# Kernel tuning notes

Hardware: AMD Instinct MI355X
Metric: run time of the kernel (lower is better)

The kernel has to match this reference:

```python
import jax, jax.numpy as jnp
import numpy as np

B, CIN, COUT, K, SDIM, H, W = 16, 512, 512, 3, 512, 64, 64


def setup_inputs() -> dict:
    key = jax.random.key(0)
    k1, k2, k3, k4 = jax.random.split(key, 4)
    return {
        "x": jax.random.normal(k1, (B, CIN, H, W), dtype=jnp.float32),
        "style": jax.random.normal(k2, (B, SDIM), dtype=jnp.float32),
        "weight": jax.random.normal(k3, (COUT, CIN, K, K), dtype=jnp.float32),
        "style_w": jax.random.normal(k4, (CIN, SDIM), dtype=jnp.float32),
        "style_b": jnp.ones((CIN,), dtype=jnp.float32),  # bias.data.fill_(1.0)
    }


def reference(x, style, weight, style_w, style_b):
    batch, in_ch, h, w_size = x.shape
    out_ch, _, ks, _ = weight.shape
    pad = ks // 2
    # EqualizedLinear: runtime weight scaling by 1/sqrt(fan_in)
    lin_scale = 1.0 / np.sqrt(style_w.shape[1])
    s = style @ (style_w * lin_scale).T + style_b  # [B, Cin]
    # modulate
    conv_scale = 1.0 / np.sqrt(in_ch * ks * ks)
    wmod = (weight[None] * conv_scale) * s[:, None, :, None, None]  # [B,Cout,Cin,k,k]
    # demodulate
    dcoef = jax.lax.rsqrt(jnp.sum(jnp.square(wmod), axis=(2, 3, 4)) + 1e-8)  # [B,Cout]
    wmod = wmod * dcoef[:, :, None, None, None]
    # grouped conv with groups = batch
    x_r = x.reshape(1, batch * in_ch, h, w_size)
    w_r = wmod.reshape(batch * out_ch, in_ch, ks, ks)
    out = jax.lax.conv_general_dilated(
        x_r, w_r,
        window_strides=(1, 1),
        padding=[(pad, pad), (pad, pad)],
        dimension_numbers=("NCHW", "OIHW", "NCHW"),
        feature_group_count=batch,
    )
    return out.reshape(batch, out_ch, h, w_size)
```

## Files before the change

kernel.cpp:

```cpp
#include <hip/hip_runtime.h>
#include <math.h>

#define B 16
#define CIN 512
#define COUT 512
#define SDIM 512
#define H 64
#define W 64

typedef short s16x8 __attribute__((ext_vector_type(8)));
typedef float f32x4 __attribute__((ext_vector_type(4)));

__device__ __constant__ float LIN_SCALE  = 0.04419417382415922f;
__device__ __constant__ float CONV_SCALE = 0.014731391274719742f;

__device__ __forceinline__ ushort f2bf(float f) {
  unsigned u = __float_as_uint(f);
  return (ushort)((u + 0x7FFFu + ((u >> 16) & 1u)) >> 16);
}

#define GLOAD16(g, l)                                           \
  __builtin_amdgcn_global_load_lds(                             \
      (const __attribute__((address_space(1))) unsigned*)(g),   \
      (__attribute__((address_space(3))) unsigned*)(l), 16, 0, 0)

__global__ __launch_bounds__(512) void style_mod_kernel(
    const float* __restrict__ style, const float* __restrict__ style_w,
    const float* __restrict__ style_b, float* __restrict__ s,
    float* __restrict__ s2) {
  const int b = blockIdx.x;
  const int ci = threadIdx.x;
  __shared__ float st[SDIM];
  st[ci] = style[b * SDIM + ci];
  __syncthreads();

  const float4* wr = reinterpret_cast<const float4*>(style_w + (size_t)ci * SDIM);
  float acc = 0.f;
#pragma unroll 4
  for (int k = 0; k < SDIM / 4; ++k) {
    float4 wv = wr[k];
    acc += st[4 * k + 0] * wv.x + st[4 * k + 1] * wv.y +
           st[4 * k + 2] * wv.z + st[4 * k + 3] * wv.w;
  }
  float v = acc * LIN_SCALE + style_b[ci];
  s[b * CIN + ci] = v;
  s2[b * CIN + ci] = v * v;
}

__global__ __launch_bounds__(256) void wsq_kernel(
    const float* __restrict__ weight, float* __restrict__ wsq) {
  const int i = blockIdx.x * blockDim.x + threadIdx.x;
  if (i >= COUT * CIN) return;
  const float* p = weight + (size_t)i * 9;
  float a = 0.f;
#pragma unroll
  for (int k = 0; k < 9; ++k) {
    float v = p[k];
    a += v * v;
  }
  wsq[i] = a;
}

__global__ __launch_bounds__(512) void dcoef_kernel(
    const float* __restrict__ s2, const float* __restrict__ wsq,
    float* __restrict__ outscale) {
  const int b = blockIdx.x;
  const int co = threadIdx.x;
  __shared__ float sh[CIN];
  sh[co] = s2[b * CIN + co];
  __syncthreads();

  const float4* wr = reinterpret_cast<const float4*>(wsq + (size_t)co * CIN);
  float acc = 0.f;
#pragma unroll 4
  for (int k = 0; k < CIN / 4; ++k) {
    float4 wv = wr[k];
    acc += sh[4 * k + 0] * wv.x + sh[4 * k + 1] * wv.y +
           sh[4 * k + 2] * wv.z + sh[4 * k + 3] * wv.w;
  }
  float d = rsqrtf(acc * CONV_SCALE * CONV_SCALE + 1e-8f);
  outscale[b * COUT + co] = d * CONV_SCALE;
}

__global__ __launch_bounds__(256) void pack_w_kernel(
    const float* __restrict__ w, ushort* __restrict__ wt) {
  const int t = blockIdx.x * 256 + threadIdx.x;
  const int s = t & 3;
  const int chunk = (t >> 2) & 15;
  const int co = t >> 6;
  const float4* wp =
      (const float4*)(w + ((size_t)co * 512 + chunk * 32 + s * 8) * 9);
  float wv[72];
#pragma unroll
  for (int i = 0; i < 18; ++i) {
    float4 v = wp[i];
    wv[4 * i + 0] = v.x; wv[4 * i + 1] = v.y;
    wv[4 * i + 2] = v.z; wv[4 * i + 3] = v.w;
  }
  const int sp = s ^ ((co >> 1) & 3);
  ushort* dst = wt + (size_t)chunk * 147456 + (size_t)co * 32 + sp * 8;
#pragma unroll
  for (int j = 0; j < 9; ++j) {
    s16x8 p;
#pragma unroll
    for (int i = 0; i < 8; ++i) p[i] = (short)f2bf(wv[i * 9 + j]);
    *(s16x8*)(dst + (size_t)j * 16384) = p;
  }
}

__global__ __launch_bounds__(256) void pack_x_kernel(
    const float* __restrict__ x, const float* __restrict__ smod,
    ushort* __restrict__ xp) {
  __shared__ float xt[32][65];
  __shared__ float sm[32];
  const int tid = threadIdx.x;
  const int gr = blockIdx.x, chunk = blockIdx.y, b = blockIdx.z;
  if (tid < 32) sm[tid] = smod[b * 512 + chunk * 32 + tid];
  {
    const int ci = tid >> 3, cq = tid & 7;
    const float4* rp = (const float4*)(
        x + (((size_t)b * 512 + chunk * 32 + ci) * 64 + gr) * 64 + cq * 8);
    float4 a = rp[0], c2 = rp[1];
    float* row = &xt[ci][cq * 8];
    row[0] = a.x; row[1] = a.y; row[2] = a.z; row[3] = a.w;
    row[4] = c2.x; row[5] = c2.y; row[6] = c2.z; row[7] = c2.w;
  }
  __syncthreads();
  const int c = tid >> 2, s = tid & 3;
  s16x8 p;
#pragma unroll
  for (int i = 0; i < 8; ++i)
    p[i] = (short)f2bf(xt[s * 8 + i][c] * sm[s * 8 + i]);
  const int sp = s ^ (((c + 1) >> 1) & 3);
  *(s16x8*)(xp + ((size_t)(b * 16 + chunk) * 64 + gr) * 2048 + c * 32 + sp * 8) = p;
}

#define WSBUF 36864
#define XSBUF 42240
#define XSOFF 73728

__global__ __launch_bounds__(512, 2) void conv_mfma3_kernel(
    const ushort* __restrict__ wt, const ushort* __restrict__ xp,
    const float* __restrict__ outscale, float* __restrict__ out) {
  extern __shared__ char smem[];

  const int tid = threadIdx.x;
  const int hb = blockIdx.x;
  const int cb = blockIdx.y;
  const int b  = blockIdx.z;
  const int h0 = hb * 8, co0 = cb * 64;
  const int lane = tid & 63, wid = tid >> 6;
  const int l15 = lane & 15, l4 = lane >> 4;

  {
    s16x8* p = (s16x8*)(smem + XSOFF);
    for (int e = tid; e < (2 * XSBUF) / 16; e += 512) p[e] = (s16x8)0;
  }

  f32x4 acc[4][4];
#pragma unroll
  for (int mt = 0; mt < 4; ++mt)
#pragma unroll
    for (int nt = 0; nt < 4; ++nt) acc[mt][nt] = (f32x4)0.f;

  const int am = (l4 ^ ((l15 >> 1) & 3)) * 16;
  int aoff[4];
#pragma unroll
  for (int mt = 0; mt < 4; ++mt) aoff[mt] = (mt * 16 + l15) * 64 + am;
  int boff[12];
#pragma unroll
  for (int nt = 0; nt < 4; ++nt)
#pragma unroll
    for (int kw = 0; kw < 3; ++kw) {
      int col = nt * 16 + l15 + kw;
      boff[nt * 3 + kw] =
          wid * 4224 + col * 64 + ((l4 ^ ((col >> 1) & 3)) * 16);
    }

  const char* wsrc0 = (const char*)wt + cb * 4096 + lane * 16;
  const char* xsrc0 = (const char*)xp + (size_t)b * 4194304 + lane * 16;

  __syncthreads();

  auto stage = [&](int chunk, int buf) {
    const char* wsrc = wsrc0 + (size_t)chunk * 294912;
    const char* xsrc = xsrc0 + (size_t)chunk * 262144;
    char* wdst = smem + buf * WSBUF + lane * 16;
    char* xdst = smem + XSOFF + buf * XSBUF + 64 + lane * 16;
    for (int e = wid; e < 76; e += 8) {
      if (e < 36) {
        int j = e >> 2, q = e & 3;
        GLOAD16(wsrc + j * 32768 + q * 1024, wdst + j * 4096 + q * 1024);
      } else {
        int r = (e - 36) >> 2, q = (e - 36) & 3;
        int gr = h0 - 1 + r;
        if ((unsigned)gr < 64u)
          GLOAD16(xsrc + (size_t)gr * 4096 + q * 1024,
                  xdst + r * 4224 + q * 1024);
      }
    }
  };

  auto compute = [&](int buf) {
    const char* wb = smem + buf * WSBUF;
    const char* xb = smem + XSOFF + buf * XSBUF;
#pragma unroll
    for (int kh = 0; kh < 3; ++kh) {
      const char* xrow = xb + kh * 4224;
#pragma unroll
      for (int kw = 0; kw < 3; ++kw) {
        const int j = kh * 3 + kw;
        const char* wj = wb + j * 4096;
        s16x8 af[4], bf[4];
#pragma unroll
        for (int mt = 0; mt < 4; ++mt)
          af[mt] = *(const s16x8*)(wj + aoff[mt]);
#pragma unroll
        for (int nt = 0; nt < 4; ++nt)
          bf[nt] = *(const s16x8*)(xrow + boff[nt * 3 + kw]);
#pragma unroll
        for (int mt = 0; mt < 4; ++mt)
#pragma unroll
          for (int nt = 0; nt < 4; ++nt)
            acc[mt][nt] = __builtin_amdgcn_mfma_f32_16x16x32_bf16(
                af[mt], bf[nt], acc[mt][nt], 0, 0, 0);
      }
    }
  };

  stage(0, 0);
  for (int c = 0; c < 16; c += 2) {
    __syncthreads();
    if (c + 1 < 16) stage(c + 1, 1);
    compute(0);
    __syncthreads();
    if (c + 2 < 16) stage(c + 2, 0);
    compute(1);
  }

  const int h = h0 + wid;
#pragma unroll
  for (int mt = 0; mt < 4; ++mt) {
#pragma unroll
    for (int r = 0; r < 4; ++r) {
      const int co = co0 + mt * 16 + l4 * 4 + r;
      const float osc = outscale[b * COUT + co];
      float* orow = out + (((size_t)b * COUT + co) * H + h) * W;
#pragma unroll
      for (int nt = 0; nt < 4; ++nt)
        orow[nt * 16 + l15] = acc[mt][nt][r] * osc;
    }
  }
}

__global__ __launch_bounds__(256, 2) void conv_mfma2_kernel(
    const ushort* __restrict__ wt, const ushort* __restrict__ xp,
    const float* __restrict__ outscale, float* __restrict__ out) {
  __shared__ ushort ws[9][64][32];
  __shared__ ushort xs[6][66][32];

  const int tid = threadIdx.x;
  const int hb = blockIdx.x, cb = blockIdx.y, b = blockIdx.z;
  const int h0 = hb * 4, co0 = cb * 64;
  const int lane = tid & 63, wid = tid >> 6;
  const int l15 = lane & 15, l4 = lane >> 4;

  {
    s16x8* p = (s16x8*)&xs[0][0][0];
    for (int e = tid; e < 1584; e += 256) p[e] = (s16x8)0;
  }

  f32x4 acc[4][4];
#pragma unroll
  for (int mt = 0; mt < 4; ++mt)
#pragma unroll
    for (int nt = 0; nt < 4; ++nt) acc[mt][nt] = (f32x4)0.f;

  const int am = (l4 ^ ((l15 >> 1) & 3)) * 16;
  int aoff[4];
#pragma unroll
  for (int mt = 0; mt < 4; ++mt) aoff[mt] = (mt * 16 + l15) * 64 + am;
  int boff[12];
#pragma unroll
  for (int nt = 0; nt < 4; ++nt)
#pragma unroll
    for (int kw = 0; kw < 3; ++kw) {
      int col = nt * 16 + l15 + kw;
      boff[nt * 3 + kw] =
          wid * 4224 + col * 64 + ((l4 ^ ((col >> 1) & 3)) * 16);
    }

  const char* wsrc0 = (const char*)wt + cb * 4096 + wid * 1024 + lane * 16;
  const char* xsrc0 =
      (const char*)xp + (size_t)b * 4194304 + wid * 1024 + lane * 16;
  char* wdst = (char*)&ws[0][0][0] + wid * 1024 + lane * 16;
  char* xdst = (char*)&xs[0][0][0] + 64 + wid * 1024 + lane * 16;

  __syncthreads();

  for (int chunk = 0; chunk < 16; ++chunk) {
    const char* wsrc = wsrc0 + chunk * 294912;
    const char* xsrc = xsrc0 + chunk * 262144;
#pragma unroll
    for (int t = 0; t < 9; ++t)
      GLOAD16(wsrc + t * 32768, wdst + t * 4096);
#pragma unroll
    for (int t = 0; t < 6; ++t) {
      int gr = h0 - 1 + t;
      if ((unsigned)gr < 64u) GLOAD16(xsrc + gr * 4096, xdst + t * 4224);
    }
    __syncthreads();

#pragma unroll
    for (int kh = 0; kh < 3; ++kh) {
      const char* xrow = (const char*)&xs[0][0][0] + kh * 4224;
#pragma unroll
      for (int kw = 0; kw < 3; ++kw) {
        const int j = kh * 3 + kw;
        const char* wj = (const char*)&ws[0][0][0] + j * 4096;
        s16x8 af[4], bf[4];
#pragma unroll
        for (int mt = 0; mt < 4; ++mt)
          af[mt] = *(const s16x8*)(wj + aoff[mt]);
#pragma unroll
        for (int nt = 0; nt < 4; ++nt)
          bf[nt] = *(const s16x8*)(xrow + boff[nt * 3 + kw]);
#pragma unroll
        for (int mt = 0; mt < 4; ++mt)
#pragma unroll
          for (int nt = 0; nt < 4; ++nt)
            acc[mt][nt] = __builtin_amdgcn_mfma_f32_16x16x32_bf16(
                af[mt], bf[nt], acc[mt][nt], 0, 0, 0);
      }
    }
    __syncthreads();
  }

  const int h = h0 + wid;
#pragma unroll
  for (int mt = 0; mt < 4; ++mt) {
#pragma unroll
    for (int r = 0; r < 4; ++r) {
      const int co = co0 + mt * 16 + l4 * 4 + r;
      const float osc = outscale[b * COUT + co];
      float* orow = out + (((size_t)b * COUT + co) * H + h) * W;
#pragma unroll
      for (int nt = 0; nt < 4; ++nt)
        orow[nt * 16 + l15] = acc[mt][nt][r] * osc;
    }
  }
}

extern "C" void kernel_launch(void* const* d_in, const int* in_sizes, int n_in,
                              void* d_out, int out_size, void* d_ws,
                              size_t ws_size, hipStream_t stream) {
  const float* x = (const float*)d_in[0];
  const float* style = (const float*)d_in[1];
  const float* weight = (const float*)d_in[2];
  const float* style_w = (const float*)d_in[3];
  const float* style_b = (const float*)d_in[4];
  float* out = (float*)d_out;

  char* wsb = (char*)d_ws;
  float* s = (float*)(wsb + 0);
  float* s2 = (float*)(wsb + 32768);
  float* wsq = (float*)(wsb + 65536);
  float* outscale = (float*)(wsb + 1114112);
  ushort* wt = (ushort*)(wsb + 1146880);
  ushort* xp = (ushort*)(wsb + 5865472);
  const size_t NEED = 72974336;

  style_mod_kernel<<<B, 512, 0, stream>>>(style, style_w, style_b, s, s2);
  wsq_kernel<<<(COUT * CIN + 255) / 256, 256, 0, stream>>>(weight, wsq);
  dcoef_kernel<<<B, 512, 0, stream>>>(s2, wsq, outscale);

  pack_w_kernel<<<128, 256, 0, stream>>>(weight, wt);
  pack_x_kernel<<<dim3(64, 16, 16), 256, 0, stream>>>(x, s, xp);

  const int DLDS = 2 * WSBUF + 2 * XSBUF;
  static_assert(2 * WSBUF + 2 * XSBUF == 158208, "lds layout");
  hipError_t attr_ok = hipFuncSetAttribute(
      reinterpret_cast<const void*>(conv_mfma3_kernel),
      hipFuncAttributeMaxDynamicSharedMemorySize, DLDS);

  if (attr_ok == hipSuccess && ws_size >= NEED) {
    conv_mfma3_kernel<<<dim3(8, 8, 16), 512, DLDS, stream>>>(wt, xp, outscale,
                                                             out);
  } else {
    conv_mfma2_kernel<<<dim3(16, 8, 16), 256, 0, stream>>>(wt, xp, outscale,
                                                           out);
  }
}
```

Baseline: 363.6 us.

## Give each wave two output rows and drop LDS double buffering in conv kernel

The conv kernel goes from 512 threads (8 waves, one output row each) with double-buffered LDS to 256 threads (4 waves, two output rows each) with a single LDS buffer. Each weight fragment loaded from LDS is now reused across two rows, and LDS use roughly halves, which should let more blocks fit per CU. The cost is that global-to-LDS loads no longer overlap compute within a block, since each chunk is loaded, synced, computed and synced again. Register pressure also rises from doubling the accumulators.

```diff
diff --git a/kernel.cpp b/kernel.cpp
--- a/kernel.cpp
+++ b/kernel.cpp
@@ -135,11 +135,10 @@
   *(s16x8*)(xp + ((size_t)(b * 16 + chunk) * 64 + gr) * 2048 + c * 32 + sp * 8) = p;
 }
 
-#define WSBUF 36864
-#define XSBUF 42240
-#define XSOFF 73728
-
-__global__ __launch_bounds__(512, 2) void conv_mfma3_kernel(
+#define XS4OFF 36864
+#define DLDS4 79104
+
+__global__ __launch_bounds__(256, 2) void conv_mfma4_kernel(
     const ushort* __restrict__ wt, const ushort* __restrict__ xp,
     const float* __restrict__ outscale, float* __restrict__ out) {
   extern __shared__ char smem[];
@@ -153,102 +152,97 @@
   const int l15 = lane & 15, l4 = lane >> 4;
 
   {
-    s16x8* p = (s16x8*)(smem + XSOFF);
-    for (int e = tid; e < (2 * XSBUF) / 16; e += 512) p[e] = (s16x8)0;
-  }
-
-  f32x4 acc[4][4];
-#pragma unroll
-  for (int mt = 0; mt < 4; ++mt)
-#pragma unroll
-    for (int nt = 0; nt < 4; ++nt) acc[mt][nt] = (f32x4)0.f;
+    s16x8* p = (s16x8*)(smem + XS4OFF);
+    for (int e = tid; e < 2640; e += 256) p[e] = (s16x8)0;
+  }
+
+  f32x4 acc[2][4][4];
+#pragma unroll
+  for (int rr = 0; rr < 2; ++rr)
+#pragma unroll
+    for (int mt = 0; mt < 4; ++mt)
+#pragma unroll
+      for (int nt = 0; nt < 4; ++nt) acc[rr][mt][nt] = (f32x4)0.f;
 
   const int am = (l4 ^ ((l15 >> 1) & 3)) * 16;
   int aoff[4];
 #pragma unroll
   for (int mt = 0; mt < 4; ++mt) aoff[mt] = (mt * 16 + l15) * 64 + am;
-  int boff[12];
+  int bcol[12];
 #pragma unroll
   for (int nt = 0; nt < 4; ++nt)
 #pragma unroll
     for (int kw = 0; kw < 3; ++kw) {
       int col = nt * 16 + l15 + kw;
-      boff[nt * 3 + kw] =
-          wid * 4224 + col * 64 + ((l4 ^ ((col >> 1) & 3)) * 16);
-    }
-
-  const char* wsrc0 = (const char*)wt + cb * 4096 + lane * 16;
-  const char* xsrc0 = (const char*)xp + (size_t)b * 4194304 + lane * 16;
-
-  __syncthreads();
-
-  auto stage = [&](int chunk, int buf) {
+      bcol[nt * 3 + kw] = col * 64 + ((l4 ^ ((col >> 1) & 3)) * 16);
+    }
+
+  const char* wsrc0 = (const char*)wt + cb * 4096 + tid * 16;
+  const char* xsrc0 = (const char*)xp + (size_t)b * 4194304 + tid * 16;
+  char* wdst = smem + tid * 16;
+  char* xdst = smem + XS4OFF + 64 + tid * 16;
+  const char* wb = smem;
+  const char* xb = smem + XS4OFF + 2 * wid * 4224;
+
+  __syncthreads();
+
+  for (int chunk = 0; chunk < 16; ++chunk) {
     const char* wsrc = wsrc0 + (size_t)chunk * 294912;
     const char* xsrc = xsrc0 + (size_t)chunk * 262144;
-    char* wdst = smem + buf * WSBUF + lane * 16;
-    char* xdst = smem + XSOFF + buf * XSBUF + 64 + lane * 16;
-    for (int e = wid; e < 76; e += 8) {
-      if (e < 36) {
-        int j = e >> 2, q = e & 3;
-        GLOAD16(wsrc + j * 32768 + q * 1024, wdst + j * 4096 + q * 1024);
-      } else {
-        int r = (e - 36) >> 2, q = (e - 36) & 3;
-        int gr = h0 - 1 + r;
-        if ((unsigned)gr < 64u)
-          GLOAD16(xsrc + (size_t)gr * 4096 + q * 1024,
-                  xdst + r * 4224 + q * 1024);
-      }
-    }
-  };
-
-  auto compute = [&](int buf) {
-    const char* wb = smem + buf * WSBUF;
-    const char* xb = smem + XSOFF + buf * XSBUF;
+#pragma unroll
+    for (int t = 0; t < 9; ++t)
+      GLOAD16(wsrc + t * 32768, wdst + t * 4096);
+#pragma unroll
+    for (int t = 0; t < 10; ++t) {
+      int gr = h0 - 1 + t;
+      if ((unsigned)gr < 64u)
+        GLOAD16(xsrc + (size_t)gr * 4096, xdst + t * 4224);
+    }
+    __syncthreads();
+
 #pragma unroll
     for (int kh = 0; kh < 3; ++kh) {
-      const char* xrow = xb + kh * 4224;
 #pragma unroll
       for (int kw = 0; kw < 3; ++kw) {
         const int j = kh * 3 + kw;
         const char* wj = wb + j * 4096;
-        s16x8 af[4], bf[4];
+        s16x8 af[4], bf[2][4];
 #pragma unroll
         for (int mt = 0; mt < 4; ++mt)
           af[mt] = *(const s16x8*)(wj + aoff[mt]);
 #pragma unroll
+        for (int rr = 0; rr < 2; ++rr)
+#pragma unroll
+          for (int nt = 0; nt < 4; ++nt)
+            bf[rr][nt] =
+                *(const s16x8*)(xb + (rr + kh) * 4224 + bcol[nt * 3 + kw]);
+#pragma unroll
+        for (int rr = 0; rr < 2; ++rr)
+#pragma unroll
+          for (int mt = 0; mt < 4; ++mt)
+#pragma unroll
+            for (int nt = 0; nt < 4; ++nt)
+              acc[rr][mt][nt] = __builtin_amdgcn_mfma_f32_16x16x32_bf16(
+                  af[mt], bf[rr][nt], acc[rr][mt][nt], 0, 0, 0);
+      }
+    }
+    __syncthreads();
+  }
+
+#pragma unroll
+  for (int rr = 0; rr < 2; ++rr) {
+    const int h = h0 + 2 * wid + rr;
+#pragma unroll
+    for (int mt = 0; mt < 4; ++mt) {
+#pragma unroll
+      for (int r = 0; r < 4; ++r) {
+        const int co = co0 + mt * 16 + l4 * 4 + r;
+        const float osc = outscale[b * COUT + co];
+        float* orow = out + (((size_t)b * COUT + co) * H + h) * W;
+#pragma unroll
         for (int nt = 0; nt < 4; ++nt)
-          bf[nt] = *(const s16x8*)(xrow + boff[nt * 3 + kw]);
-#pragma unroll
-        for (int mt = 0; mt < 4; ++mt)
-#pragma unroll
-          for (int nt = 0; nt < 4; ++nt)
-            acc[mt][nt] = __builtin_amdgcn_mfma_f32_16x16x32_bf16(
-                af[mt], bf[nt], acc[mt][nt], 0, 0, 0);
+          orow[nt * 16 + l15] = acc[rr][mt][nt][r] * osc;
       }
-    }
-  };
-
-  stage(0, 0);
-  for (int c = 0; c < 16; c += 2) {
-    __syncthreads();
-    if (c + 1 < 16) stage(c + 1, 1);
-    compute(0);
-    __syncthreads();
-    if (c + 2 < 16) stage(c + 2, 0);
-    compute(1);
-  }
-
-  const int h = h0 + wid;
-#pragma unroll
-  for (int mt = 0; mt < 4; ++mt) {
-#pragma unroll
-    for (int r = 0; r < 4; ++r) {
-      const int co = co0 + mt * 16 + l4 * 4 + r;
-      const float osc = outscale[b * COUT + co];
-      float* orow = out + (((size_t)b * COUT + co) * H + h) * W;
-#pragma unroll
-      for (int nt = 0; nt < 4; ++nt)
-        orow[nt * 16 + l15] = acc[mt][nt][r] * osc;
     }
   }
 }
@@ -377,15 +371,13 @@
   pack_w_kernel<<<128, 256, 0, stream>>>(weight, wt);
   pack_x_kernel<<<dim3(64, 16, 16), 256, 0, stream>>>(x, s, xp);
 
-  const int DLDS = 2 * WSBUF + 2 * XSBUF;
-  static_assert(2 * WSBUF + 2 * XSBUF == 158208, "lds layout");
   hipError_t attr_ok = hipFuncSetAttribute(
-      reinterpret_cast<const void*>(conv_mfma3_kernel),
-      hipFuncAttributeMaxDynamicSharedMemorySize, DLDS);
+      reinterpret_cast<const void*>(conv_mfma4_kernel),
+      hipFuncAttributeMaxDynamicSharedMemorySize, DLDS4);
 
   if (attr_ok == hipSuccess && ws_size >= NEED) {
-    conv_mfma3_kernel<<<dim3(8, 8, 16), 512, DLDS, stream>>>(wt, xp, outscale,
-                                                             out);
+    conv_mfma4_kernel<<<dim3(8, 8, 16), 256, DLDS4, stream>>>(wt, xp, outscale,
+                                                              out);
   } else {
     conv_mfma2_kernel<<<dim3(16, 8, 16), 256, 0, stream>>>(wt, xp, outscale,
                                                            out);
```

After: 340.7 us. 6.3% less time.
